# Kernel optimization log

Measured on AMD Instinct MI355X. Metric: run time of the kernel, lower is better.

## Reference

```python
import jax, jax.numpy as jnp
import numpy as np

B, T, C = 2, 2048, 2048
NH, DH, DHR, L = 16, 128, 64, 512
BASE = 10000.0


def _rope_tables(t, d):
    # freq starts at 1 (faithful to source: jnp.arange(1, T+1))
    freq = jnp.arange(1, t + 1, dtype=jnp.float32)[:, None]          # [t,1]
    pos = jnp.repeat(jnp.arange(d // 2, dtype=jnp.float32), 2)[None]  # [1,d]
    theta = jnp.exp(-pos / d * jnp.log(BASE))
    return jnp.cos(freq * theta), jnp.sin(freq * theta)               # [t,d]


def _rope(x, t_start=0):
    # x: [B, t, d]; interleaved-pair rotation
    b, t, d = x.shape
    cos, sin = _rope_tables(t_start + t, d)
    cos, sin = cos[t_start:t_start + t], sin[t_start:t_start + t]
    xf = x.astype(jnp.float32)
    xr = xf.reshape(b, t, d // 2, 2)
    rot = jnp.stack([-xr[..., 1], xr[..., 0]], axis=-1).reshape(b, t, d)
    return (xf * cos + rot * sin).astype(x.dtype)


def setup_inputs() -> dict:
    key = jax.random.key(0)
    ks = jax.random.split(key, 13)
    s = 0.02
    return {
        "x":   jax.random.normal(ks[0], (B, T, C), jnp.float32),
        "WA":  jax.random.normal(ks[1], (C, 2 * L), jnp.float32) * s,
        "bA":  jnp.zeros((2 * L,), jnp.float32),
        "WB":  jax.random.normal(ks[2], (2 * L, DHR), jnp.float32) * s,
        "bB":  jnp.zeros((DHR,), jnp.float32),
        "WC":  jax.random.normal(ks[3], (2 * L, DHR * NH), jnp.float32) * s,
        "bC":  jnp.zeros((DHR * NH,), jnp.float32),
        "WUQ": jax.random.normal(ks[4], (L, NH * DH), jnp.float32) * s,
        "WUK": jax.random.normal(ks[5], (L, NH * DH), jnp.float32) * s,
        "WUV": jax.random.normal(ks[6], (L, NH * DH), jnp.float32) * s,
        "WZ":  jax.random.normal(ks[7], (NH * DH, C), jnp.float32) * s,
        "bZ":  jnp.zeros((C,), jnp.float32),
    }


def reference(x, WA, bA, WB, bB, WC, bC, WUQ, WUK, WUV, WZ, bZ):
    b, t, _ = x.shape
    h = x @ WA + bA                                  # [b,t,2L]
    kv_lat, q_lat = jnp.split(h, 2, axis=-1)         # [b,t,L] each

    # decoupled RoPE branch
    kRt = _rope(h @ WB + bB, 0)                      # [b,t,DHR] shared across heads
    qRt = _rope(h @ WC + bC, 0)                      # [b,t,NH*DHR]
    qRt = qRt.reshape(b, t, NH, DHR).transpose(0, 2, 1, 3)  # [b,nh,t,DHR]

    # up-projections from latents
    q = (q_lat @ WUQ).reshape(b, t, NH, DH).transpose(0, 2, 1, 3)
    k = (kv_lat @ WUK).reshape(b, t, NH, DH).transpose(0, 2, 1, 3)
    v = (kv_lat @ WUV).reshape(b, t, NH, DH).transpose(0, 2, 1, 3)

    qf = jnp.concatenate([q, qRt], axis=-1)                            # [b,nh,t,DH+DHR]
    kf = jnp.concatenate([k, jnp.broadcast_to(kRt[:, None], (b, NH, t, DHR))], axis=-1)

    dk = DH + DHR
    scores = jnp.einsum("bhqd,bhkd->bhqk", qf.astype(jnp.float32), kf.astype(jnp.float32)) * dk ** -0.5
    causal = jnp.tril(jnp.ones((t, t), dtype=bool))
    scores = jnp.where(causal, scores, -jnp.inf)
    attn = jax.nn.softmax(scores, axis=-1)
    out = jnp.einsum("bhqk,bhkd->bhqd", attn, v.astype(jnp.float32)).astype(x.dtype)
    out = out.transpose(0, 2, 1, 3).reshape(b, t, NH * DH)
    return out @ WZ + bZ
```

## Files before the change

kernel.cpp:

```cpp
#include <hip/hip_runtime.h>
#include <hip/hip_bf16.h>
#include <math.h>


constexpr int BB  = 2;
constexpr int TT  = 2048;
constexpr int NHH = 16;
constexpr int MM  = BB * TT;
constexpr float QSCALE = 0.07216878364870323f;

typedef __attribute__((ext_vector_type(8))) short short8;
typedef __attribute__((ext_vector_type(16))) float f32x16;

__device__ __forceinline__ unsigned pk2(float lo, float hi) {
  __hip_bfloat162 h = __float22bfloat162_rn(make_float2(lo, hi));
  union { __hip_bfloat162 b; unsigned u; } cv;
  cv.b = h;
  return cv.u;
}
__device__ __forceinline__ ushort bfu(float x) {
  union { __hip_bfloat16 b; ushort u; } cv;
  cv.b = __float2bfloat16(x);
  return cv.u;
}
__device__ __forceinline__ float bf2f(ushort u) {
  union { float f; unsigned i; } cv;
  cv.i = ((unsigned)u) << 16;
  return cv.f;
}
__device__ __forceinline__ void gload_lds16(const void* g, void* l) {
  __builtin_amdgcn_global_load_lds((const __attribute__((address_space(1))) void*)g,
                                   (__attribute__((address_space(3))) void*)l, 16, 0, 0);
}

__global__ __launch_bounds__(256) void conv_kernel(const float* __restrict__ src,
                                                   ushort* __restrict__ dst) {
  const size_t i = ((size_t)blockIdx.x * 256 + threadIdx.x) * 4;
  const float4 v = *(const float4*)(src + i);
  uint2 u;
  u.x = pk2(v.x, v.y);
  u.y = pk2(v.z, v.w);
  *(uint2*)(dst + i) = u;
}

__global__ __launch_bounds__(256) void tconv_kernel(const float* __restrict__ src,
                                                    ushort* __restrict__ dst,
                                                    int K, int N) {
  __shared__ ushort tile[64][72];
  const int k0 = blockIdx.y * 64, n0 = blockIdx.x * 64;
  const int t = threadIdx.x;
  const int r = t >> 4, c4 = (t & 15) * 4;
#pragma unroll
  for (int p = 0; p < 4; ++p) {
    const int k = r + p * 16;
    const float4 v = *(const float4*)(src + (size_t)(k0 + k) * N + n0 + c4);
    tile[c4 + 0][k] = bfu(v.x);
    tile[c4 + 1][k] = bfu(v.y);
    tile[c4 + 2][k] = bfu(v.z);
    tile[c4 + 3][k] = bfu(v.w);
  }
  __syncthreads();
#pragma unroll
  for (int p = 0; p < 4; ++p) {
    const int n = r + p * 16;
    ushort4 o;
    o.x = tile[n][c4 + 0];
    o.y = tile[n][c4 + 1];
    o.z = tile[n][c4 + 2];
    o.w = tile[n][c4 + 3];
    *(ushort4*)(dst + (size_t)(n0 + n) * K + k0 + c4) = o;
  }
}

template <int RD, int OM>
__global__ __launch_bounds__(256) void gemm_mfma_kernel(
    const ushort* __restrict__ A, int lda, const ushort* __restrict__ Bt,
    const float* __restrict__ bias, void* __restrict__ Co, int N, int K) {
  __shared__ ushort As[128 * 64];
  __shared__ ushort Bs[128 * 64];
  const int tid = threadIdx.x;
  const int lane = tid & 63, wid = tid >> 6;
  const int wm = wid >> 1, wn = wid & 1;
  const int l31 = lane & 31, hl = lane >> 5;
  const int bm = blockIdx.y * 128, bn = blockIdx.x * 128;

  f32x16 acc[2][2];
#pragma unroll
  for (int mt = 0; mt < 2; ++mt)
#pragma unroll
    for (int nt = 0; nt < 2; ++nt)
#pragma unroll
      for (int r = 0; r < 16; ++r) acc[mt][nt][r] = 0.f;

  for (int k0 = 0; k0 < K; k0 += 64) {
    __syncthreads();
#pragma unroll
    for (int p = 0; p < 4; ++p) {
      const int v = tid + p * 256;
      const int r = v >> 3, sl = (v & 7) ^ (r & 7);
      gload_lds16(A + (size_t)(bm + r) * lda + k0 + sl * 8, As + v * 8);
    }
#pragma unroll
    for (int p = 0; p < 4; ++p) {
      const int v = tid + p * 256;
      const int r = v >> 3, sl = (v & 7) ^ (r & 7);
      gload_lds16(Bt + (size_t)(bn + r) * K + k0 + sl * 8, Bs + v * 8);
    }
    __syncthreads();
#pragma unroll
    for (int ks = 0; ks < 4; ++ks) {
      short8 af[2], bf[2];
      const int cb = ks * 32 + hl * 16;
#pragma unroll
      for (int mt = 0; mt < 2; ++mt) {
        const int row = wm * 64 + mt * 32 + l31;
        af[mt] = *(const short8*)((const char*)As + row * 128 + (cb ^ ((row & 7) << 4)));
      }
#pragma unroll
      for (int nt = 0; nt < 2; ++nt) {
        const int col = wn * 64 + nt * 32 + l31;
        bf[nt] = *(const short8*)((const char*)Bs + col * 128 + (cb ^ ((col & 7) << 4)));
      }
#pragma unroll
      for (int mt = 0; mt < 2; ++mt)
#pragma unroll
        for (int nt = 0; nt < 2; ++nt)
          acc[mt][nt] = __builtin_amdgcn_mfma_f32_32x32x16_bf16(af[mt], bf[nt],
                                                                acc[mt][nt], 0, 0, 0);
    }
  }

  const float kinv = (RD != 0) ? (9.210340371976184f / (float)RD) : 0.f;
#pragma unroll
  for (int mt = 0; mt < 2; ++mt)
#pragma unroll
    for (int nt = 0; nt < 2; ++nt) {
      const int col = bn + wn * 64 + nt * 32 + l31;
      const float bi = bias ? bias[col] : 0.f;
      float th = 0.f;
      if constexpr (RD != 0) th = expf(-(float)(col >> 1) * kinv);
#pragma unroll
      for (int r = 0; r < 16; ++r) {
        const int row = bm + wm * 64 + mt * 32 + ((r & 3) + 8 * (r >> 2) + 4 * hl);
        float v = acc[mt][nt][r] + bi;
        if constexpr (RD != 0) {
          const int t = row & (TT - 1);
          float sn, cs;
          sincosf((float)(t + 1) * th, &sn, &cs);
          const float pv = __shfl_xor(v, 1);
          v = (l31 & 1) ? (v * cs + pv * sn) : (v * cs - pv * sn);
        }
        if constexpr (OM == 2) v *= QSCALE;
        if constexpr (OM == 0)
          ((float*)Co)[(size_t)row * N + col] = v;
        else
          ((ushort*)Co)[(size_t)row * N + col] = bfu(v);
      }
    }
}

__global__ __launch_bounds__(256) void gemm64_kernel(
    const ushort* __restrict__ A, int lda, const float* __restrict__ W,
    const float* __restrict__ bias, ushort* __restrict__ Co, int N, int K) {
  __shared__ float As[16][68];
  __shared__ float Bs[16][68];
  const int tid = threadIdx.x;
  const int tx = tid & 15, ty = tid >> 4;
  const int bm = blockIdx.y * 64;
  float acc[4][4] = {};

  for (int k0 = 0; k0 < K; k0 += 16) {
    const ushort4 au = *(const ushort4*)(A + (size_t)(bm + (tid >> 2)) * lda + k0 + (tid & 3) * 4);
    const float4 bv = *(const float4*)(W + (size_t)(k0 + (tid >> 4)) * N + (tid & 15) * 4);
    __syncthreads();
    const int ak = (tid & 3) * 4, arr = tid >> 2;
    As[ak + 0][arr] = bf2f(au.x);
    As[ak + 1][arr] = bf2f(au.y);
    As[ak + 2][arr] = bf2f(au.z);
    As[ak + 3][arr] = bf2f(au.w);
    *(float4*)&Bs[tid >> 4][(tid & 15) * 4] = bv;
    __syncthreads();
#pragma unroll
    for (int k = 0; k < 16; ++k) {
      const float4 a = *(const float4*)&As[k][ty * 4];
      const float4 b = *(const float4*)&Bs[k][tx * 4];
      const float avv[4] = {a.x, a.y, a.z, a.w};
      const float bvv[4] = {b.x, b.y, b.z, b.w};
#pragma unroll
      for (int ii = 0; ii < 4; ++ii)
#pragma unroll
        for (int jj = 0; jj < 4; ++jj) acc[ii][jj] += avv[ii] * bvv[jj];
    }
  }

  const int c0 = tx * 4;
  const float4 bi = *(const float4*)(bias + c0);
  const float kinv = 9.210340371976184f / 64.0f;
  const float th0 = expf(-(float)(c0 >> 1) * kinv);
  const float th1 = expf(-(float)((c0 >> 1) + 1) * kinv);
#pragma unroll
  for (int ii = 0; ii < 4; ++ii) {
    const int r = bm + ty * 4 + ii;
    const int t = r & (TT - 1);
    float4 v = make_float4(acc[ii][0] + bi.x, acc[ii][1] + bi.y,
                           acc[ii][2] + bi.z, acc[ii][3] + bi.w);
    float s0, c0_, s1, c1_;
    sincosf((float)(t + 1) * th0, &s0, &c0_);
    sincosf((float)(t + 1) * th1, &s1, &c1_);
    const float4 o = make_float4(v.x * c0_ - v.y * s0, v.y * c0_ + v.x * s0,
                                 v.z * c1_ - v.w * s1, v.w * c1_ + v.z * s1);
    uint2 u;
    u.x = pk2(o.x, o.y);
    u.y = pk2(o.z, o.w);
    *(uint2*)(Co + (size_t)r * N + c0) = u;
  }
}

__global__ __launch_bounds__(256, 2) void flash_kernel(
    const ushort* __restrict__ qarr, const ushort* __restrict__ qRarr,
    const ushort* __restrict__ karr, const ushort* __restrict__ kRarr,
    const ushort* __restrict__ varr, ushort* __restrict__ oarr) {
  __shared__ ushort Ks[64][200];
  __shared__ ushort Vt[128][72];

  const int bi = (int)gridDim.x - 1 - (int)blockIdx.x;
  const int qt0 = bi * 128;
  const int bh = blockIdx.y;
  const int b = bh >> 4, hh = bh & 15;
  const int tid = threadIdx.x;
  const int lane = tid & 63, wid = tid >> 6;
  const int l31 = lane & 31, hl = lane >> 5;
  const int qbase = qt0 + wid * 32;
  const size_t rowbase = (size_t)b * TT;

  short8 qf[12];
  {
    const ushort* qp  = qarr  + (rowbase + qbase + l31) * 2048 + hh * 128;
    const ushort* qRp = qRarr + (rowbase + qbase + l31) * 1024 + hh * 64;
#pragma unroll
    for (int ks = 0; ks < 12; ++ks) {
      const int d = ks * 16 + hl * 8;
      const ushort* p = (d < 128) ? (qp + d) : (qRp + (d - 128));
      qf[ks] = *(const short8*)p;
    }
  }

  f32x16 oacc[4];
#pragma unroll
  for (int nt = 0; nt < 4; ++nt)
#pragma unroll
    for (int r = 0; r < 16; ++r) oacc[nt][r] = 0.f;
  float m_run = -1e30f, l_run = 0.f;

  const int nkt = 2 * bi + 2;
  for (int kt = 0; kt < nkt; ++kt) {
    const int kt0 = kt * 64;
    short8 kreg[6], vreg[4];
    {
      const int r = tid >> 2, sub = tid & 3;
      const ushort* kp  = karr  + (rowbase + kt0 + r) * 2048 + hh * 128;
      const ushort* kRp = kRarr + (rowbase + kt0 + r) * 64;
#pragma unroll
      for (int c = 0; c < 6; ++c) {
        const int d0 = c * 32 + sub * 8;
        const ushort* p = (d0 < 128) ? (kp + d0) : (kRp + (d0 - 128));
        kreg[c] = *(const short8*)p;
      }
      const int vr = tid & 63, dblk = tid >> 6;
      const ushort* vp = varr + (rowbase + kt0 + vr) * 2048 + hh * 128 + dblk * 32;
#pragma unroll
      for (int c = 0; c < 4; ++c) vreg[c] = *(const short8*)(vp + c * 8);
    }
    __syncthreads();
    {
      const int r = tid >> 2, sub = tid & 3;
#pragma unroll
      for (int c = 0; c < 6; ++c) *(short8*)&Ks[r][c * 32 + sub * 8] = kreg[c];
      const int vr = tid & 63, dblk = tid >> 6;
#pragma unroll
      for (int c = 0; c < 4; ++c)
#pragma unroll
        for (int e = 0; e < 8; ++e)
          Vt[dblk * 32 + c * 8 + e][vr] = (ushort)vreg[c][e];
    }
    __syncthreads();

    if (kt0 < qbase + 32) {
      f32x16 sa[2];
#pragma unroll
      for (int t2 = 0; t2 < 2; ++t2)
#pragma unroll
        for (int r = 0; r < 16; ++r) sa[t2][r] = 0.f;
#pragma unroll
      for (int ks = 0; ks < 12; ++ks) {
        const short8 ka0 = *(const short8*)&Ks[l31][ks * 16 + hl * 8];
        const short8 ka1 = *(const short8*)&Ks[32 + l31][ks * 16 + hl * 8];
        sa[0] = __builtin_amdgcn_mfma_f32_32x32x16_bf16(ka0, qf[ks], sa[0], 0, 0, 0);
        sa[1] = __builtin_amdgcn_mfma_f32_32x32x16_bf16(ka1, qf[ks], sa[1], 0, 0, 0);
      }
      if (kt0 + 63 > qbase) {
        const int qrow = qbase + l31;
#pragma unroll
        for (int t2 = 0; t2 < 2; ++t2)
#pragma unroll
          for (int r = 0; r < 16; ++r) {
            const int kcol = kt0 + t2 * 32 + (r & 3) + 8 * (r >> 2) + 4 * hl;
            if (kcol > qrow) sa[t2][r] = -1e30f;
          }
      }
      float pmax = -1e30f;
#pragma unroll
      for (int t2 = 0; t2 < 2; ++t2)
#pragma unroll
        for (int r = 0; r < 16; ++r) pmax = fmaxf(pmax, sa[t2][r]);
      pmax = fmaxf(pmax, __shfl_xor(pmax, 32));
      if (!__all(pmax <= m_run + 8.0f)) {
        const float mnew = fmaxf(m_run, pmax);
        const float alpha = __expf(m_run - mnew);
        m_run = mnew;
        l_run *= alpha;
#pragma unroll
        for (int r = 0; r < 16; ++r) {
          const int qr = (r & 3) + 8 * (r >> 2) + 4 * hl;
          const float al = __shfl(alpha, qr);
          oacc[0][r] *= al; oacc[1][r] *= al; oacc[2][r] *= al; oacc[3][r] *= al;
        }
      }
      float rsum = 0.f;
#pragma unroll
      for (int t2 = 0; t2 < 2; ++t2)
#pragma unroll
        for (int r = 0; r < 16; ++r) {
          const float p = __expf(sa[t2][r] - m_run);
          sa[t2][r] = p;
          rsum += p;
        }
      rsum += __shfl_xor(rsum, 32);
      l_run += rsum;
      short8 pf[4];
#pragma unroll
      for (int t2 = 0; t2 < 2; ++t2)
#pragma unroll
        for (int kb = 0; kb < 2; ++kb) {
          const int g = kb * 8;
          unsigned wa = pk2(sa[t2][g + 0], sa[t2][g + 1]);
          unsigned wb = pk2(sa[t2][g + 4], sa[t2][g + 5]);
          unsigned wc = pk2(sa[t2][g + 2], sa[t2][g + 3]);
          unsigned wd = pk2(sa[t2][g + 6], sa[t2][g + 7]);
          asm volatile("v_permlane32_swap_b32 %0, %1" : "+v"(wa), "+v"(wb));
          asm volatile("v_permlane32_swap_b32 %0, %1" : "+v"(wc), "+v"(wd));
          union { unsigned u[4]; short8 s; } cv;
          cv.u[0] = wa; cv.u[1] = wc; cv.u[2] = wb; cv.u[3] = wd;
          pf[t2 * 2 + kb] = cv.s;
        }
#pragma unroll
      for (int ks = 0; ks < 4; ++ks)
#pragma unroll
        for (int nt = 0; nt < 4; ++nt) {
          const short8 vf = *(const short8*)&Vt[nt * 32 + l31][ks * 16 + hl * 8];
          oacc[nt] = __builtin_amdgcn_mfma_f32_32x32x16_bf16(pf[ks], vf, oacc[nt], 0, 0, 0);
        }
    }
  }

  const float inv = 1.0f / l_run;
#pragma unroll
  for (int r = 0; r < 16; ++r) {
    const int qr = (r & 3) + 8 * (r >> 2) + 4 * hl;
    const float il = __shfl(inv, qr);
    ushort* orow = oarr + (rowbase + qbase + qr) * 2048 + hh * 128;
#pragma unroll
    for (int nt = 0; nt < 4; ++nt) orow[nt * 32 + l31] = bfu(oacc[nt][r] * il);
  }
}

extern "C" void kernel_launch(void* const* d_in, const int* in_sizes, int n_in,
                              void* d_out, int out_size, void* d_ws, size_t ws_size,
                              hipStream_t stream) {
  const float* x   = (const float*)d_in[0];
  const float* WA  = (const float*)d_in[1];
  const float* bA  = (const float*)d_in[2];
  const float* WB  = (const float*)d_in[3];
  const float* bB  = (const float*)d_in[4];
  const float* WC  = (const float*)d_in[5];
  const float* bC  = (const float*)d_in[6];
  const float* WUQ = (const float*)d_in[7];
  const float* WUK = (const float*)d_in[8];
  const float* WUV = (const float*)d_in[9];
  const float* WZ  = (const float*)d_in[10];
  const float* bZ  = (const float*)d_in[11];
  float* out = (float*)d_out;

  ushort* xb   = (ushort*)d_ws;
  ushort* WAt  = xb   + (size_t)MM * 2048;
  ushort* WCt  = WAt  + (size_t)1024 * 2048;
  ushort* WUQt = WCt  + (size_t)1024 * 1024;
  ushort* WUKt = WUQt + (size_t)2048 * 512;
  ushort* WUVt = WUKt + (size_t)2048 * 512;
  ushort* WZt  = WUVt + (size_t)2048 * 512;
  ushort* hb   = WZt  + (size_t)2048 * 2048;
  ushort* kR   = hb   + (size_t)MM * 1024;
  ushort* qR   = kR   + (size_t)MM * 64;
  ushort* qb   = qR   + (size_t)MM * 1024;
  ushort* kb   = qb   + (size_t)MM * 2048;
  ushort* vb   = kb   + (size_t)MM * 2048;
  ushort* aob  = vb   + (size_t)MM * 2048;

  const dim3 thr(256);

  conv_kernel<<<dim3((MM * 2048) / 1024), thr, 0, stream>>>(x, xb);
  tconv_kernel<<<dim3(1024 / 64, 2048 / 64), thr, 0, stream>>>(WA, WAt, 2048, 1024);
  tconv_kernel<<<dim3(1024 / 64, 1024 / 64), thr, 0, stream>>>(WC, WCt, 1024, 1024);
  tconv_kernel<<<dim3(2048 / 64, 512 / 64), thr, 0, stream>>>(WUQ, WUQt, 512, 2048);
  tconv_kernel<<<dim3(2048 / 64, 512 / 64), thr, 0, stream>>>(WUK, WUKt, 512, 2048);
  tconv_kernel<<<dim3(2048 / 64, 512 / 64), thr, 0, stream>>>(WUV, WUVt, 512, 2048);
  tconv_kernel<<<dim3(2048 / 64, 2048 / 64), thr, 0, stream>>>(WZ, WZt, 2048, 2048);

  gemm_mfma_kernel<0, 1><<<dim3(1024 / 128, MM / 128), thr, 0, stream>>>(
      xb, 2048, WAt, bA, hb, 1024, 2048);
  gemm64_kernel<<<dim3(1, MM / 64), thr, 0, stream>>>(hb, 1024, WB, bB, kR, 64, 1024);
  gemm_mfma_kernel<1024, 2><<<dim3(1024 / 128, MM / 128), thr, 0, stream>>>(
      hb, 1024, WCt, bC, qR, 1024, 1024);
  gemm_mfma_kernel<0, 2><<<dim3(2048 / 128, MM / 128), thr, 0, stream>>>(
      hb + 512, 1024, WUQt, nullptr, qb, 2048, 512);
  gemm_mfma_kernel<0, 1><<<dim3(2048 / 128, MM / 128), thr, 0, stream>>>(
      hb, 1024, WUKt, nullptr, kb, 2048, 512);
  gemm_mfma_kernel<0, 1><<<dim3(2048 / 128, MM / 128), thr, 0, stream>>>(
      hb, 1024, WUVt, nullptr, vb, 2048, 512);
  flash_kernel<<<dim3(TT / 128, BB * NHH), thr, 0, stream>>>(qb, qR, kb, kR, vb, aob);
  gemm_mfma_kernel<0, 0><<<dim3(2048 / 128, MM / 128), thr, 0, stream>>>(
      aob, 2048, WZt, bZ, out, 2048, 2048);
}
```

Baseline: 523.1 us.

## Double-buffer GEMM LDS, move WB projection to MFMA, prefetch KV in flash

The MFMA GEMM now double-buffers its LDS tiles, so the next K-slab loads while the current one computes, and it gains a BN template to support a 64-wide N tile. The scalar fp32 WB GEMM is replaced by the MFMA GEMM using a transposed bf16 WB, with RoPE applied in the epilogue. The flash kernel prefetches the next K/V tile into registers during compute, raises wave priority around the MFMA blocks, and asks for 3 blocks per CU. The costs are more LDS and registers per block, which may limit occupancy or cause spills, and bf16 rounding of WB.

```diff
diff --git a/kernel.cpp b/kernel.cpp
--- a/kernel.cpp
+++ b/kernel.cpp
@@ -22,11 +22,6 @@
   union { __hip_bfloat16 b; ushort u; } cv;
   cv.b = __float2bfloat16(x);
   return cv.u;
-}
-__device__ __forceinline__ float bf2f(ushort u) {
-  union { float f; unsigned i; } cv;
-  cv.i = ((unsigned)u) << 16;
-  return cv.f;
 }
 __device__ __forceinline__ void gload_lds16(const void* g, void* l) {
   __builtin_amdgcn_global_load_lds((const __attribute__((address_space(1))) void*)g,
@@ -72,70 +67,84 @@
   }
 }
 
-template <int RD, int OM>
-__global__ __launch_bounds__(256) void gemm_mfma_kernel(
+template <int RD, int OM, int BN>
+__global__ __launch_bounds__(256, 2) void gemm_mfma_kernel(
     const ushort* __restrict__ A, int lda, const ushort* __restrict__ Bt,
     const float* __restrict__ bias, void* __restrict__ Co, int N, int K) {
-  __shared__ ushort As[128 * 64];
-  __shared__ ushort Bs[128 * 64];
+  constexpr int NT = BN / 64;
+  __shared__ ushort As[2][128 * 64];
+  __shared__ ushort Bs[2][BN * 64];
   const int tid = threadIdx.x;
   const int lane = tid & 63, wid = tid >> 6;
   const int wm = wid >> 1, wn = wid & 1;
   const int l31 = lane & 31, hl = lane >> 5;
-  const int bm = blockIdx.y * 128, bn = blockIdx.x * 128;
-
-  f32x16 acc[2][2];
+  const int bm = blockIdx.y * 128, bn = blockIdx.x * BN;
+
+  f32x16 acc[2][NT];
 #pragma unroll
   for (int mt = 0; mt < 2; ++mt)
 #pragma unroll
-    for (int nt = 0; nt < 2; ++nt)
+    for (int nt = 0; nt < NT; ++nt)
 #pragma unroll
       for (int r = 0; r < 16; ++r) acc[mt][nt][r] = 0.f;
 
-  for (int k0 = 0; k0 < K; k0 += 64) {
-    __syncthreads();
+  auto stage = [&](int buf, int k0) {
 #pragma unroll
     for (int p = 0; p < 4; ++p) {
       const int v = tid + p * 256;
       const int r = v >> 3, sl = (v & 7) ^ (r & 7);
-      gload_lds16(A + (size_t)(bm + r) * lda + k0 + sl * 8, As + v * 8);
-    }
-#pragma unroll
-    for (int p = 0; p < 4; ++p) {
+      gload_lds16(A + (size_t)(bm + r) * lda + k0 + sl * 8, &As[buf][v * 8]);
+    }
+#pragma unroll
+    for (int p = 0; p < BN / 32; ++p) {
       const int v = tid + p * 256;
       const int r = v >> 3, sl = (v & 7) ^ (r & 7);
-      gload_lds16(Bt + (size_t)(bn + r) * K + k0 + sl * 8, Bs + v * 8);
-    }
-    __syncthreads();
+      gload_lds16(Bt + (size_t)(bn + r) * K + k0 + sl * 8, &Bs[buf][v * 8]);
+    }
+  };
+
+  auto kstep = [&](int cbuf, int sbuf, int t, int nk) {
+    if (t + 1 < nk) stage(sbuf, (t + 1) * 64);
 #pragma unroll
     for (int ks = 0; ks < 4; ++ks) {
-      short8 af[2], bf[2];
+      short8 af[2], bfr[NT];
       const int cb = ks * 32 + hl * 16;
 #pragma unroll
       for (int mt = 0; mt < 2; ++mt) {
         const int row = wm * 64 + mt * 32 + l31;
-        af[mt] = *(const short8*)((const char*)As + row * 128 + (cb ^ ((row & 7) << 4)));
-      }
-#pragma unroll
-      for (int nt = 0; nt < 2; ++nt) {
-        const int col = wn * 64 + nt * 32 + l31;
-        bf[nt] = *(const short8*)((const char*)Bs + col * 128 + (cb ^ ((col & 7) << 4)));
+        af[mt] = *(const short8*)((const char*)&As[cbuf][0] + row * 128 +
+                                  (cb ^ ((row & 7) << 4)));
+      }
+#pragma unroll
+      for (int nt = 0; nt < NT; ++nt) {
+        const int col = (BN == 128 ? wn * 64 + nt * 32 : wn * 32) + l31;
+        bfr[nt] = *(const short8*)((const char*)&Bs[cbuf][0] + col * 128 +
+                                   (cb ^ ((col & 7) << 4)));
       }
 #pragma unroll
       for (int mt = 0; mt < 2; ++mt)
 #pragma unroll
-        for (int nt = 0; nt < 2; ++nt)
-          acc[mt][nt] = __builtin_amdgcn_mfma_f32_32x32x16_bf16(af[mt], bf[nt],
+        for (int nt = 0; nt < NT; ++nt)
+          acc[mt][nt] = __builtin_amdgcn_mfma_f32_32x32x16_bf16(af[mt], bfr[nt],
                                                                 acc[mt][nt], 0, 0, 0);
     }
+    __syncthreads();
+  };
+
+  const int nk = K / 64;
+  stage(0, 0);
+  __syncthreads();
+  for (int t = 0; t < nk; t += 2) {
+    kstep(0, 1, t, nk);
+    kstep(1, 0, t + 1, nk);
   }
 
   const float kinv = (RD != 0) ? (9.210340371976184f / (float)RD) : 0.f;
 #pragma unroll
   for (int mt = 0; mt < 2; ++mt)
 #pragma unroll
-    for (int nt = 0; nt < 2; ++nt) {
-      const int col = bn + wn * 64 + nt * 32 + l31;
+    for (int nt = 0; nt < NT; ++nt) {
+      const int col = bn + (BN == 128 ? wn * 64 + nt * 32 : wn * 32) + l31;
       const float bi = bias ? bias[col] : 0.f;
       float th = 0.f;
       if constexpr (RD != 0) th = expf(-(float)(col >> 1) * kinv);
@@ -159,64 +168,7 @@
     }
 }
 
-__global__ __launch_bounds__(256) void gemm64_kernel(
-    const ushort* __restrict__ A, int lda, const float* __restrict__ W,
-    const float* __restrict__ bias, ushort* __restrict__ Co, int N, int K) {
-  __shared__ float As[16][68];
-  __shared__ float Bs[16][68];
-  const int tid = threadIdx.x;
-  const int tx = tid & 15, ty = tid >> 4;
-  const int bm = blockIdx.y * 64;
-  float acc[4][4] = {};
-
-  for (int k0 = 0; k0 < K; k0 += 16) {
-    const ushort4 au = *(const ushort4*)(A + (size_t)(bm + (tid >> 2)) * lda + k0 + (tid & 3) * 4);
-    const float4 bv = *(const float4*)(W + (size_t)(k0 + (tid >> 4)) * N + (tid & 15) * 4);
-    __syncthreads();
-    const int ak = (tid & 3) * 4, arr = tid >> 2;
-    As[ak + 0][arr] = bf2f(au.x);
-    As[ak + 1][arr] = bf2f(au.y);
-    As[ak + 2][arr] = bf2f(au.z);
-    As[ak + 3][arr] = bf2f(au.w);
-    *(float4*)&Bs[tid >> 4][(tid & 15) * 4] = bv;
-    __syncthreads();
-#pragma unroll
-    for (int k = 0; k < 16; ++k) {
-      const float4 a = *(const float4*)&As[k][ty * 4];
-      const float4 b = *(const float4*)&Bs[k][tx * 4];
-      const float avv[4] = {a.x, a.y, a.z, a.w};
-      const float bvv[4] = {b.x, b.y, b.z, b.w};
-#pragma unroll
-      for (int ii = 0; ii < 4; ++ii)
-#pragma unroll
-        for (int jj = 0; jj < 4; ++jj) acc[ii][jj] += avv[ii] * bvv[jj];
-    }
-  }
-
-  const int c0 = tx * 4;
-  const float4 bi = *(const float4*)(bias + c0);
-  const float kinv = 9.210340371976184f / 64.0f;
-  const float th0 = expf(-(float)(c0 >> 1) * kinv);
-  const float th1 = expf(-(float)((c0 >> 1) + 1) * kinv);
-#pragma unroll
-  for (int ii = 0; ii < 4; ++ii) {
-    const int r = bm + ty * 4 + ii;
-    const int t = r & (TT - 1);
-    float4 v = make_float4(acc[ii][0] + bi.x, acc[ii][1] + bi.y,
-                           acc[ii][2] + bi.z, acc[ii][3] + bi.w);
-    float s0, c0_, s1, c1_;
-    sincosf((float)(t + 1) * th0, &s0, &c0_);
-    sincosf((float)(t + 1) * th1, &s1, &c1_);
-    const float4 o = make_float4(v.x * c0_ - v.y * s0, v.y * c0_ + v.x * s0,
-                                 v.z * c1_ - v.w * s1, v.w * c1_ + v.z * s1);
-    uint2 u;
-    u.x = pk2(o.x, o.y);
-    u.y = pk2(o.z, o.w);
-    *(uint2*)(Co + (size_t)r * N + c0) = u;
-  }
-}
-
-__global__ __launch_bounds__(256, 2) void flash_kernel(
+__global__ __launch_bounds__(256, 3) void flash_kernel(
     const ushort* __restrict__ qarr, const ushort* __restrict__ qRarr,
     const ushort* __restrict__ karr, const ushort* __restrict__ kRarr,
     const ushort* __restrict__ varr, ushort* __restrict__ oarr) {
@@ -252,31 +204,30 @@
     for (int r = 0; r < 16; ++r) oacc[nt][r] = 0.f;
   float m_run = -1e30f, l_run = 0.f;
 
+  short8 kreg[6], vreg[4];
+  const int ldr = tid >> 2, lds4 = tid & 3;
+  const int vr = tid & 63, dblk = tid >> 6;
+  auto loadKV = [&](int kt0) {
+    const ushort* kp  = karr  + (rowbase + kt0 + ldr) * 2048 + hh * 128;
+    const ushort* kRp = kRarr + (rowbase + kt0 + ldr) * 64;
+#pragma unroll
+    for (int c = 0; c < 6; ++c) {
+      const int d0 = c * 32 + lds4 * 8;
+      const ushort* p = (d0 < 128) ? (kp + d0) : (kRp + (d0 - 128));
+      kreg[c] = *(const short8*)p;
+    }
+    const ushort* vp = varr + (rowbase + kt0 + vr) * 2048 + hh * 128 + dblk * 32;
+#pragma unroll
+    for (int c = 0; c < 4; ++c) vreg[c] = *(const short8*)(vp + c * 8);
+  };
+
   const int nkt = 2 * bi + 2;
+  loadKV(0);
   for (int kt = 0; kt < nkt; ++kt) {
-    const int kt0 = kt * 64;
-    short8 kreg[6], vreg[4];
-    {
-      const int r = tid >> 2, sub = tid & 3;
-      const ushort* kp  = karr  + (rowbase + kt0 + r) * 2048 + hh * 128;
-      const ushort* kRp = kRarr + (rowbase + kt0 + r) * 64;
-#pragma unroll
-      for (int c = 0; c < 6; ++c) {
-        const int d0 = c * 32 + sub * 8;
-        const ushort* p = (d0 < 128) ? (kp + d0) : (kRp + (d0 - 128));
-        kreg[c] = *(const short8*)p;
-      }
-      const int vr = tid & 63, dblk = tid >> 6;
-      const ushort* vp = varr + (rowbase + kt0 + vr) * 2048 + hh * 128 + dblk * 32;
-#pragma unroll
-      for (int c = 0; c < 4; ++c) vreg[c] = *(const short8*)(vp + c * 8);
-    }
     __syncthreads();
     {
-      const int r = tid >> 2, sub = tid & 3;
-#pragma unroll
-      for (int c = 0; c < 6; ++c) *(short8*)&Ks[r][c * 32 + sub * 8] = kreg[c];
-      const int vr = tid & 63, dblk = tid >> 6;
+#pragma unroll
+      for (int c = 0; c < 6; ++c) *(short8*)&Ks[ldr][c * 32 + lds4 * 8] = kreg[c];
 #pragma unroll
       for (int c = 0; c < 4; ++c)
 #pragma unroll
@@ -284,13 +235,16 @@
           Vt[dblk * 32 + c * 8 + e][vr] = (ushort)vreg[c][e];
     }
     __syncthreads();
-
+    if (kt + 1 < nkt) loadKV((kt + 1) * 64);
+
+    const int kt0 = kt * 64;
     if (kt0 < qbase + 32) {
       f32x16 sa[2];
 #pragma unroll
       for (int t2 = 0; t2 < 2; ++t2)
 #pragma unroll
         for (int r = 0; r < 16; ++r) sa[t2][r] = 0.f;
+      __builtin_amdgcn_s_setprio(1);
 #pragma unroll
       for (int ks = 0; ks < 12; ++ks) {
         const short8 ka0 = *(const short8*)&Ks[l31][ks * 16 + hl * 8];
@@ -298,6 +252,7 @@
         sa[0] = __builtin_amdgcn_mfma_f32_32x32x16_bf16(ka0, qf[ks], sa[0], 0, 0, 0);
         sa[1] = __builtin_amdgcn_mfma_f32_32x32x16_bf16(ka1, qf[ks], sa[1], 0, 0, 0);
       }
+      __builtin_amdgcn_s_setprio(0);
       if (kt0 + 63 > qbase) {
         const int qrow = qbase + l31;
 #pragma unroll
@@ -353,6 +308,7 @@
           cv.u[0] = wa; cv.u[1] = wc; cv.u[2] = wb; cv.u[3] = wd;
           pf[t2 * 2 + kb] = cv.s;
         }
+      __builtin_amdgcn_s_setprio(1);
 #pragma unroll
       for (int ks = 0; ks < 4; ++ks)
 #pragma unroll
@@ -360,6 +316,7 @@
           const short8 vf = *(const short8*)&Vt[nt * 32 + l31][ks * 16 + hl * 8];
           oacc[nt] = __builtin_amdgcn_mfma_f32_32x32x16_bf16(pf[ks], vf, oacc[nt], 0, 0, 0);
         }
+      __builtin_amdgcn_s_setprio(0);
     }
   }
 
@@ -405,29 +362,32 @@
   ushort* kb   = qb   + (size_t)MM * 2048;
   ushort* vb   = kb   + (size_t)MM * 2048;
   ushort* aob  = vb   + (size_t)MM * 2048;
+  ushort* WBt  = aob  + (size_t)MM * 2048;
 
   const dim3 thr(256);
 
   conv_kernel<<<dim3((MM * 2048) / 1024), thr, 0, stream>>>(x, xb);
   tconv_kernel<<<dim3(1024 / 64, 2048 / 64), thr, 0, stream>>>(WA, WAt, 2048, 1024);
   tconv_kernel<<<dim3(1024 / 64, 1024 / 64), thr, 0, stream>>>(WC, WCt, 1024, 1024);
+  tconv_kernel<<<dim3(64 / 64, 1024 / 64), thr, 0, stream>>>(WB, WBt, 1024, 64);
   tconv_kernel<<<dim3(2048 / 64, 512 / 64), thr, 0, stream>>>(WUQ, WUQt, 512, 2048);
   tconv_kernel<<<dim3(2048 / 64, 512 / 64), thr, 0, stream>>>(WUK, WUKt, 512, 2048);
   tconv_kernel<<<dim3(2048 / 64, 512 / 64), thr, 0, stream>>>(WUV, WUVt, 512, 2048);
   tconv_kernel<<<dim3(2048 / 64, 2048 / 64), thr, 0, stream>>>(WZ, WZt, 2048, 2048);
 
-  gemm_mfma_kernel<0, 1><<<dim3(1024 / 128, MM / 128), thr, 0, stream>>>(
+  gemm_mfma_kernel<0, 1, 128><<<dim3(1024 / 128, MM / 128), thr, 0, stream>>>(
       xb, 2048, WAt, bA, hb, 1024, 2048);
-  gemm64_kernel<<<dim3(1, MM / 64), thr, 0, stream>>>(hb, 1024, WB, bB, kR, 64, 1024);
-  gemm_mfma_kernel<1024, 2><<<dim3(1024 / 128, MM / 128), thr, 0, stream>>>(
+  gemm_mfma_kernel<64, 1, 64><<<dim3(1, MM / 128), thr, 0, stream>>>(
+      hb, 1024, WBt, bB, kR, 64, 1024);
+  gemm_mfma_kernel<1024, 2, 128><<<dim3(1024 / 128, MM / 128), thr, 0, stream>>>(
       hb, 1024, WCt, bC, qR, 1024, 1024);
-  gemm_mfma_kernel<0, 2><<<dim3(2048 / 128, MM / 128), thr, 0, stream>>>(
+  gemm_mfma_kernel<0, 2, 128><<<dim3(2048 / 128, MM / 128), thr, 0, stream>>>(
       hb + 512, 1024, WUQt, nullptr, qb, 2048, 512);
-  gemm_mfma_kernel<0, 1><<<dim3(2048 / 128, MM / 128), thr, 0, stream>>>(
+  gemm_mfma_kernel<0, 1, 128><<<dim3(2048 / 128, MM / 128), thr, 0, stream>>>(
       hb, 1024, WUKt, nullptr, kb, 2048, 512);
-  gemm_mfma_kernel<0, 1><<<dim3(2048 / 128, MM / 128), thr, 0, stream>>>(
+  gemm_mfma_kernel<0, 1, 128><<<dim3(2048 / 128, MM / 128), thr, 0, stream>>>(
       hb, 1024, WUVt, nullptr, vb, 2048, 512);
   flash_kernel<<<dim3(TT / 128, BB * NHH), thr, 0, stream>>>(qb, qR, kb, kR, vb, aob);
-  gemm_mfma_kernel<0, 0><<<dim3(2048 / 128, MM / 128), thr, 0, stream>>>(
+  gemm_mfma_kernel<0, 0, 128><<<dim3(2048 / 128, MM / 128), thr, 0, stream>>>(
       aob, 2048, WZt, bZ, out, 2048, 2048);
 }
```

New measurement: 592.3 us. +13.2%, slower.
